# Performance work log

Measured on AMD Instinct MI355X. Metric: run time of the kernel, lower is better.

Reference implementation:

```python
import jax, jax.numpy as jnp
import numpy as np

B, TXT_T, MEL_T, N_MEL = 8, 200, 800, 80
PAD_MAG = 1.0e12


def setup_inputs() -> dict:
    key = jax.random.key(0)
    k1, k2, k3, k4 = jax.random.split(key, 4)
    mu_logvar = jax.random.normal(k1, (B, TXT_T, 2 * N_MEL), dtype=jnp.float32)
    melspec = jax.random.normal(k2, (B, N_MEL, MEL_T), dtype=jnp.float32)
    # lengths are 1-based (indexed as length-1), keep them in [T//2, T]
    text_lengths = jax.random.randint(k3, (B,), TXT_T // 2, TXT_T + 1)
    mel_lengths = jax.random.randint(k4, (B,), MEL_T // 2, MEL_T + 1)
    return {
        "mu_logvar": mu_logvar,
        "melspec": melspec,
        "text_lengths": text_lengths,
        "mel_lengths": mel_lengths,
    }


def _log_prob_matrix(mu_logvar, melspec):
    # melspec: [B, n_mel, mel_T] -> x: [B, 1, mel_T, n_mel]
    x = jnp.transpose(melspec, (0, 2, 1))[:, None, :, :]
    mu = mu_logvar[:, :, :N_MEL][:, :, None, :]       # [B, txt_T, 1, n_mel]
    logvar = mu_logvar[:, :, N_MEL:][:, :, None, :]   # [B, txt_T, 1, n_mel]
    # -0.5 * mean_over_mel( (x-mu)^2 / exp(logvar) + logvar )
    sq = (x - mu) ** 2
    return (-0.5 * (sq * jnp.exp(-logvar) + logvar)).mean(axis=3)  # [B, txt_T, mel_T]


def reference(mu_logvar, melspec, text_lengths, mel_lengths):
    lp = _log_prob_matrix(mu_logvar, melspec)  # [B, txt_T, mel_T]

    # log_alpha column carry, with a leading pad row (index 0 stays -PAD_MAG)
    init = jnp.full((B, TXT_T + 1), -PAD_MAG, dtype=lp.dtype)
    init = init.at[:, 1].set(lp[:, 0, 0])

    def step(a, lp_t):  # a: [B, txt_T+1], lp_t: [B, txt_T]
        # logsumexp over {stay, advance}; original adds 1e-7 to prev values
        new_rows = jnp.logaddexp(a[:, 1:] + 1e-7, a[:, :-1] + 1e-7) + lp_t
        a = a.at[:, 1:].set(new_rows)
        return a, new_rows

    lp_rest = jnp.moveaxis(lp[:, :, 1:], 2, 0)  # [mel_T-1, B, txt_T]
    _, cols = jax.lax.scan(step, init, lp_rest)  # cols: [mel_T-1, B, txt_T]

    log_alpha = jnp.concatenate(
        [init[:, 1:, None], jnp.moveaxis(cols, 0, 2)], axis=2
    )  # [B, txt_T, mel_T]

    b = jnp.arange(B)
    alpha_last = log_alpha[b, text_lengths - 1, mel_lengths - 1]
    alpha_last = alpha_last / mel_lengths.astype(alpha_last.dtype)
    mdn_loss = -alpha_last.mean()
    return mdn_loss, lp
```

## Files before the change

### kernel.cpp

```cpp
#include <hip/hip_runtime.h>
#include <math.h>

#define BB 8
#define TXT_T 200
#define MEL_T 800
#define N_MEL 80
#define LPT_STRIDE 200
#define LOG2E 1.44269504088896340736f
#define LN2   0.69314718055994530942f
#define EPS2  (1e-7f * LOG2E)
#define NPAD  -1.0e12f

__device__ __forceinline__ float exp2_hw(float x) {
#if __has_builtin(__builtin_amdgcn_exp2f)
    return __builtin_amdgcn_exp2f(x);
#else
    return __expf(LN2 * x);
#endif
}

__device__ __forceinline__ float lse2(float A, float B) {
    float m = fmaxf(A, B);
    float e = exp2_hw(-fabsf(A - B));
    return m + __log2f(1.0f + e);
}

__device__ __forceinline__ float lse3(float A, float B, float C) {
    float m = fmaxf(fmaxf(A, B), C);
    float e = exp2_hw(A - m) + exp2_hw(B - m) + exp2_hw(C - m);
    return m + __log2f(e);
}

__global__ void __launch_bounds__(256) lp_kernel(
        const float* __restrict__ mu_logvar,
        const float* __restrict__ melspec,
        float* __restrict__ out_lp,
        float* __restrict__ lpT) {
    const int bt = blockIdx.x;
    const int b  = bt / TXT_T;
    const int t  = bt % TXT_T;
    const int tid = threadIdx.x;

    __shared__ float s_mu[N_MEL];
    __shared__ float s_ev[N_MEL];
    __shared__ float s_lv[N_MEL];
    __shared__ float s_sumlv;

    if (tid < N_MEL) {
        float mu = mu_logvar[(size_t)bt * (2 * N_MEL) + tid];
        float lv = mu_logvar[(size_t)bt * (2 * N_MEL) + N_MEL + tid];
        s_mu[tid] = mu;
        s_ev[tid] = __expf(-lv);
        s_lv[tid] = lv;
    }
    __syncthreads();
    if (tid == 0) {
        float s = 0.f;
        #pragma unroll
        for (int n = 0; n < N_MEL; ++n) s += s_lv[n];
        s_sumlv = s;
    }
    __syncthreads();

    if (tid < MEL_T / 4) {
        const float4* ms4 = (const float4*)(melspec + (size_t)b * N_MEL * MEL_T);
        float ax = 0.f, ay = 0.f, az = 0.f, aw = 0.f;
        #pragma unroll 8
        for (int n = 0; n < N_MEL; ++n) {
            float4 x = ms4[(size_t)n * (MEL_T / 4) + tid];
            float mu = s_mu[n];
            float ev = s_ev[n];
            float d0 = x.x - mu; ax += d0 * d0 * ev;
            float d1 = x.y - mu; ay += d1 * d1 * ev;
            float d2 = x.z - mu; az += d2 * d2 * ev;
            float d3 = x.w - mu; aw += d3 * d3 * ev;
        }
        const float c = -0.5f / (float)N_MEL;
        float slv = s_sumlv;
        float l0 = c * (ax + slv);
        float l1 = c * (ay + slv);
        float l2 = c * (az + slv);
        float l3 = c * (aw + slv);

        size_t ob = (size_t)bt * MEL_T + tid * 4;
        out_lp[ob + 0] = l0;
        out_lp[ob + 1] = l1;
        out_lp[ob + 2] = l2;
        out_lp[ob + 3] = l3;

        int m0 = tid * 4;
        size_t tb = ((size_t)b * MEL_T + m0) * LPT_STRIDE + t;
        lpT[tb + 0 * LPT_STRIDE] = l0 * LOG2E + EPS2;
        lpT[tb + 1 * LPT_STRIDE] = l1 * LOG2E + EPS2;
        lpT[tb + 2 * LPT_STRIDE] = l2 * LOG2E + EPS2;
        lpT[tb + 3 * LPT_STRIDE] = l3 * LOG2E + EPS2;
    }
}

#define PF 8
#define LDR(row) (*(const float4*)(base + (size_t)(row) * LPT_STRIDE))

#define STEP2(PK, QK, TT) do {                                                \
    float4 p_ = PK; float4 q_ = QK;                                           \
    int rp_ = (TT) + 2 * PF;                                                  \
    int ra_ = rp_     > (MEL_T - 1) ? (MEL_T - 1) : rp_;                      \
    int rb_ = rp_ + 1 > (MEL_T - 1) ? (MEL_T - 1) : rp_ + 1;                  \
    PK = LDR(ra_); QK = LDR(rb_);                                             \
    float l1_ = __shfl_up(r3, 1);                                             \
    float l2_ = __shfl_up(r2, 1);                                             \
    float pw_ = __shfl_up(p_.w, 1);                                           \
    if (lane == 0) { l1_ = NPAD; l2_ = NPAD; pw_ = NPAD; }                    \
    if ((TT) == myMel) {          \
        float ga_ = r0, gb_ = l1_, gp_ = p_.x;                                \
        if (acomp == 1) { ga_ = r1; gb_ = r0; gp_ = p_.y; }                   \
        if (acomp == 2) { ga_ = r2; gb_ = r1; gp_ = p_.z; }                   \
        if (acomp == 3) { ga_ = r3; gb_ = r2; gp_ = p_.w; }                   \
        alpha_out[b] = (lse2(ga_, gb_) + gp_) * scale;                        \
    }                                                                         \
    float s0_ = lse2(p_.x, pw_);                                              \
    float s1_ = lse2(p_.y, p_.x);                                             \
    float s2_ = lse2(p_.z, p_.y);                                             \
    float s3_ = lse2(p_.w, p_.z);                                             \
    float x0_ = r0 + p_.x, x1_ = r1 + p_.y, x2_ = r2 + p_.z, x3_ = r3 + p_.w; \
    float y0_ = l1_ + s0_, y1_ = r0 + s1_, y2_ = r1 + s2_, y3_ = r2 + s3_;    \
    float z0_ = l2_ + pw_, z1_ = l1_ + p_.x, z2_ = r0 + p_.y, z3_ = r1 + p_.z;\
    r0 = lse3(x0_, y0_, z0_) + q_.x;                                          \
    r1 = lse3(x1_, y1_, z1_) + q_.y;                                          \
    r2 = lse3(x2_, y2_, z2_) + q_.z;                                          \
    r3 = lse3(x3_, y3_, z3_) + q_.w;                                          \
    if ((TT) + 1 == myMel) {          \
        float v_ = r0;                                                        \
        if (acomp == 1) v_ = r1;                                              \
        if (acomp == 2) v_ = r2;                                              \
        if (acomp == 3) v_ = r3;                                              \
        alpha_out[b] = v_ * scale;                                            \
    }                                                                         \
} while (0)

__global__ void __launch_bounds__(64) scan_kernel(
        const float* __restrict__ lpT,
        const int* __restrict__ text_lengths,
        const int* __restrict__ mel_lengths,
        float* __restrict__ alpha_out) {
    const int b = blockIdx.x;
    const int lane = threadIdx.x;
    int j0 = lane * 4;
    j0 = j0 > (TXT_T - 4) ? (TXT_T - 4) : j0;

    const int melL1 = mel_lengths[b] - 1;
    const int txtL1 = text_lengths[b] - 1;
    const float scale = LN2 / (float)(melL1 + 1);
    const int acomp = txtL1 & 3;
    const int myMel = (lane == (txtL1 >> 2)) ? melL1 : -1;

    const float* base = lpT + (size_t)b * MEL_T * LPT_STRIDE + j0;

    float4 i0 = LDR(0);
    float r0 = (lane == 0) ? (i0.x - EPS2) : NPAD;
    float r1 = NPAD, r2 = NPAD, r3 = NPAD;

    float4 P0 = LDR(1),  Q0 = LDR(2);
    float4 P1 = LDR(3),  Q1 = LDR(4);
    float4 P2 = LDR(5),  Q2 = LDR(6);
    float4 P3 = LDR(7),  Q3 = LDR(8);
    float4 P4 = LDR(9),  Q4 = LDR(10);
    float4 P5 = LDR(11), Q5 = LDR(12);
    float4 P6 = LDR(13), Q6 = LDR(14);
    float4 P7 = LDR(15), Q7 = LDR(16);

    for (int t = 1; t <= melL1; t += 2 * PF) {
        STEP2(P0, Q0, t + 0);
        STEP2(P1, Q1, t + 2);
        STEP2(P2, Q2, t + 4);
        STEP2(P3, Q3, t + 6);
        STEP2(P4, Q4, t + 8);
        STEP2(P5, Q5, t + 10);
        STEP2(P6, Q6, t + 12);
        STEP2(P7, Q7, t + 14);
    }
}

__global__ void finish_kernel(const float* __restrict__ alpha,
                              float* __restrict__ out) {
    float s = 0.f;
    #pragma unroll
    for (int b = 0; b < BB; ++b) s += alpha[b];
    out[0] = -(s / (float)BB);
}

extern "C" void kernel_launch(void* const* d_in, const int* in_sizes, int n_in,
                              void* d_out, int out_size, void* d_ws, size_t ws_size,
                              hipStream_t stream) {
    const float* mu_logvar    = (const float*)d_in[0];
    const float* melspec      = (const float*)d_in[1];
    const int*   text_lengths = (const int*)d_in[2];
    const int*   mel_lengths  = (const int*)d_in[3];
    float* out = (float*)d_out;

    float* alpha = (float*)d_ws;
    float* lpT   = (float*)d_ws + 16;

    lp_kernel<<<BB * TXT_T, 256, 0, stream>>>(mu_logvar, melspec, out + 1, lpT);
    scan_kernel<<<BB, 64, 0, stream>>>(lpT, text_lengths, mel_lengths, alpha);
    finish_kernel<<<1, 1, 0, stream>>>(alpha, out);
}
```

Measured before the change: 156.8 us.

## Double-buffer scan kernel's lpT chunks into LDS via global_load_lds

The serial alpha scan no longer prefetches lpT rows from global memory into a ring of registers. It now streams 32-row chunks into a double-buffered shared-memory array using asynchronous global-to-LDS loads, synchronised with vmcnt waits. Each timestep then reads its two rows from LDS. This is meant to take global-load latency and register pressure off the serial dependency chain, at the cost of LDS read latency and 51 KB of shared memory per block.

```diff
diff --git a/kernel.cpp b/kernel.cpp
--- a/kernel.cpp
+++ b/kernel.cpp
@@ -6,6 +6,7 @@
 #define MEL_T 800
 #define N_MEL 80
 #define LPT_STRIDE 200
+#define CH 32
 #define LOG2E 1.44269504088896340736f
 #define LN2   0.69314718055994530942f
 #define EPS2  (1e-7f * LOG2E)
@@ -97,15 +98,19 @@
     }
 }
 
-#define PF 8
-#define LDR(row) (*(const float4*)(base + (size_t)(row) * LPT_STRIDE))
-
-#define STEP2(PK, QK, TT) do {                                                \
-    float4 p_ = PK; float4 q_ = QK;                                           \
-    int rp_ = (TT) + 2 * PF;                                                  \
-    int ra_ = rp_     > (MEL_T - 1) ? (MEL_T - 1) : rp_;                      \
-    int rb_ = rp_ + 1 > (MEL_T - 1) ? (MEL_T - 1) : rp_ + 1;                  \
-    PK = LDR(ra_); QK = LDR(rb_);                                             \
+__device__ __forceinline__ void stage_chunk(const float* g, float* s, int lane) {
+    #pragma unroll
+    for (int i = 0; i < 25; ++i) {
+        __builtin_amdgcn_global_load_lds(
+            (const __attribute__((address_space(1))) void*)(g + i * 256 + lane * 4),
+            (__attribute__((address_space(3))) void*)(s + i * 256),
+            16, 0, 0);
+    }
+}
+
+#define STEP2L(SB, TLOC, TT) do {                                             \
+    float4 p_ = *(const float4*)((SB) + (TLOC) * LPT_STRIDE + j0);            \
+    float4 q_ = *(const float4*)((SB) + ((TLOC) + 1) * LPT_STRIDE + j0);      \
     float l1_ = __shfl_up(r3, 1);                                             \
     float l2_ = __shfl_up(r2, 1);                                             \
     float pw_ = __shfl_up(p_.w, 1);                                           \
@@ -142,6 +147,7 @@
         const int* __restrict__ text_lengths,
         const int* __restrict__ mel_lengths,
         float* __restrict__ alpha_out) {
+    __shared__ float sbuf[2][CH][LPT_STRIDE];
     const int b = blockIdx.x;
     const int lane = threadIdx.x;
     int j0 = lane * 4;
@@ -153,30 +159,46 @@
     const int acomp = txtL1 & 3;
     const int myMel = (lane == (txtL1 >> 2)) ? melL1 : -1;
 
-    const float* base = lpT + (size_t)b * MEL_T * LPT_STRIDE + j0;
-
-    float4 i0 = LDR(0);
-    float r0 = (lane == 0) ? (i0.x - EPS2) : NPAD;
-    float r1 = NPAD, r2 = NPAD, r3 = NPAD;
-
-    float4 P0 = LDR(1),  Q0 = LDR(2);
-    float4 P1 = LDR(3),  Q1 = LDR(4);
-    float4 P2 = LDR(5),  Q2 = LDR(6);
-    float4 P3 = LDR(7),  Q3 = LDR(8);
-    float4 P4 = LDR(9),  Q4 = LDR(10);
-    float4 P5 = LDR(11), Q5 = LDR(12);
-    float4 P6 = LDR(13), Q6 = LDR(14);
-    float4 P7 = LDR(15), Q7 = LDR(16);
-
-    for (int t = 1; t <= melL1; t += 2 * PF) {
-        STEP2(P0, Q0, t + 0);
-        STEP2(P1, Q1, t + 2);
-        STEP2(P2, Q2, t + 4);
-        STEP2(P3, Q3, t + 6);
-        STEP2(P4, Q4, t + 8);
-        STEP2(P5, Q5, t + 10);
-        STEP2(P6, Q6, t + 12);
-        STEP2(P7, Q7, t + 14);
+    const float* gbase = lpT + (size_t)b * MEL_T * LPT_STRIDE;
+    const int clast = melL1 >> 5;
+
+    stage_chunk(gbase,                    &sbuf[0][0][0], lane);
+    stage_chunk(gbase + CH * LPT_STRIDE,  &sbuf[1][0][0], lane);
+
+    float r0 = NPAD, r1 = NPAD, r2 = NPAD, r3 = NPAD;
+
+    for (int c = 0; c <= clast; ++c) {
+        if (c < clast) { asm volatile("s_waitcnt vmcnt(25)" ::: "memory"); }
+        else           { asm volatile("s_waitcnt vmcnt(0)"  ::: "memory"); }
+
+        const float* sb = &sbuf[c & 1][0][0];
+        if (c == 0) {
+            float4 row0 = *(const float4*)(sb + j0);
+            float4 row1 = *(const float4*)(sb + LPT_STRIDE + j0);
+            r0 = (lane == 0) ? (row0.x - EPS2) : NPAD;
+            float lft = __shfl_up(r3, 1);
+            if (lane == 0) lft = NPAD;
+            float m0 = lse2(r0, lft) + row1.x;
+            float m1 = lse2(r1, r0)  + row1.y;
+            float m2 = lse2(r2, r1)  + row1.z;
+            float m3 = lse2(r3, r2)  + row1.w;
+            r0 = m0; r1 = m1; r2 = m2; r3 = m3;
+            #pragma unroll
+            for (int m = 0; m < 15; ++m) {
+                STEP2L(sb, 2 * m + 2, 2 * m + 2);
+            }
+        } else {
+            const int tbase = 32 * c;
+            #pragma unroll
+            for (int m = 0; m < 16; ++m) {
+                STEP2L(sb, 2 * m, tbase + 2 * m);
+            }
+        }
+
+        if (c + 2 <= clast) {
+            stage_chunk(gbase + (size_t)(c + 2) * CH * LPT_STRIDE,
+                        &sbuf[c & 1][0][0], lane);
+        }
     }
 }
 
```

New measurement: 156.1 us. Within noise of the previous version (-0.4%).
